# Performance work log

Hardware: AMD Instinct MI355X
Metric: run time of the kernel (lower is better)

## Reference

```python
import jax, jax.numpy as jnp
import numpy as np

B_SIZE = 4096
IN_FEATURES = 8192
OUT_FEATURES = IN_FEATURES + 6  # in + step(2) + 2*pad(2)
PAD = 2
BAND = 3  # each input column n contributes to output columns n..n+2


def setup_inputs() -> dict:
    key = jax.random.key(0)
    k1, k2, k3 = jax.random.split(key, 3)
    stdv = 1.0 / np.sqrt(IN_FEATURES)  # reset_parameters: uniform(-stdv, stdv)
    x = jax.random.normal(k1, (B_SIZE, IN_FEATURES), dtype=jnp.float32)
    weight = jax.random.uniform(k2, (OUT_FEATURES, IN_FEATURES), minval=-stdv, maxval=stdv, dtype=jnp.float32)
    bias = jax.random.uniform(k3, (OUT_FEATURES,), minval=-stdv, maxval=stdv, dtype=jnp.float32)
    return {"x": x, "weight": weight, "bias": bias}


def reference(x, weight, bias):
    # Torch loop: for n in range(F): out[:, n:n+3] += x[:, n:n+1] * weight[n:n+3, n] + bias[n:n+3]
    # => out[:, c] = sum_{n in [c-2, c] & [0, F)} x[:, n] * weight[c, n]  +  bias[c] * count(c)
    # where count(c) = number of valid n hitting column c (bias is re-added per touch).
    B, F = x.shape
    O = F + 2 * PAD + 2
    idx = jnp.arange(F)
    out = jnp.zeros((B, O), dtype=x.dtype)
    count = jnp.zeros((O,), dtype=x.dtype)
    for d in range(BAND):  # tiny fixed band, not a data-dim loop
        diag = weight[idx + d, idx]              # [F] band diagonal d
        out = out.at[:, d:d + F].add(x * diag[None, :])
        count = count.at[d:d + F].add(1.0)
    out = out + bias * count
    return out[:, PAD:-PAD]  # [B, F + 2]
```

## Files before the change

### kernel.cpp

```cpp
#include <hip/hip_runtime.h>

#define B_SIZE 4096
#define IN_F   8192
#define OUT_W  8194
#define ROWS_PER_BLOCK 16

__global__ __launch_bounds__(256) void coeff_kernel(
    const float* __restrict__ w, const float* __restrict__ bias,
    float4* __restrict__ coeff) {
  int j = blockIdx.x * blockDim.x + threadIdx.x;
  if (j >= OUT_W) return;
  size_t c = (size_t)j + 2;
  float c0 = 0.f, c1 = 0.f, c2 = 0.f, cnt = 0.f;
  if (j     < IN_F) { c0 = w[c * IN_F + j    ]; cnt += 1.f; }
  if (j + 1 < IN_F) { c1 = w[c * IN_F + j + 1]; cnt += 1.f; }
  if (j + 2 < IN_F) { c2 = w[c * IN_F + j + 2]; cnt += 1.f; }
  coeff[j] = make_float4(c0, c1, c2, cnt * bias[c]);
}

__global__ __launch_bounds__(256) void band_kernel(
    const float* __restrict__ x, const float4* __restrict__ coeff,
    float* __restrict__ out) {
  const int j = (blockIdx.x * 256 + threadIdx.x) * 4;
  const float4 k0 = coeff[j];
  const float4 k1 = coeff[j + 1];
  const float4 k2 = coeff[j + 2];
  const float4 k3 = coeff[j + 3];
  const bool g4 = (j + 4 < IN_F);
  const bool g5 = (j + 5 < IN_F);
  const bool tail = (blockIdx.x == gridDim.x - 1) && (threadIdx.x < 2);
  const int row0 = blockIdx.y * ROWS_PER_BLOCK;

  #pragma unroll 4
  for (int r = 0; r < ROWS_PER_BLOCK; ++r) {
    const size_t row = (size_t)(row0 + r);
    const float* xr = x + row * (size_t)IN_F;
    float4 xv = *reinterpret_cast<const float4*>(xr + j);
    float x4 = g4 ? xr[j + 4] : 0.f;
    float x5 = g5 ? xr[j + 5] : 0.f;
    float4 o;
    o.x = fmaf(k0.x, xv.x, fmaf(k0.y, xv.y, fmaf(k0.z, xv.z, k0.w)));
    o.y = fmaf(k1.x, xv.y, fmaf(k1.y, xv.z, fmaf(k1.z, xv.w, k1.w)));
    o.z = fmaf(k2.x, xv.z, fmaf(k2.y, xv.w, fmaf(k2.z, x4,  k2.w)));
    o.w = fmaf(k3.x, xv.w, fmaf(k3.y, x4,  fmaf(k3.z, x5,  k3.w)));
    float* orow = out + row * (size_t)OUT_W + j;
    reinterpret_cast<float2*>(orow)[0] = make_float2(o.x, o.y);
    reinterpret_cast<float2*>(orow)[1] = make_float2(o.z, o.w);
    if (tail) out[row * (size_t)OUT_W + 8192 + threadIdx.x] = 0.f;
  }
}

extern "C" void kernel_launch(void* const* d_in, const int* in_sizes, int n_in,
                              void* d_out, int out_size, void* d_ws, size_t ws_size,
                              hipStream_t stream) {
  const float* x    = (const float*)d_in[0];
  const float* w    = (const float*)d_in[1];
  const float* bias = (const float*)d_in[2];
  float* out = (float*)d_out;
  float4* coeff = (float4*)d_ws;

  coeff_kernel<<<(OUT_W + 255) / 256, 256, 0, stream>>>(w, bias, coeff);

  dim3 grid(8, B_SIZE / ROWS_PER_BLOCK);
  band_kernel<<<grid, 256, 0, stream>>>(x, coeff, out);
}
```

Before: 63.29 us.

## Fuse coefficient gather into band kernel, shuffle neighbors, double rows per block

```diff
diff --git a/kernel.cpp b/kernel.cpp
--- a/kernel.cpp
+++ b/kernel.cpp
@@ -3,50 +3,57 @@
 #define B_SIZE 4096
 #define IN_F   8192
 #define OUT_W  8194
-#define ROWS_PER_BLOCK 16
+#define ROWS   32
+#define CHUNKS 8
 
-__global__ __launch_bounds__(256) void coeff_kernel(
-    const float* __restrict__ w, const float* __restrict__ bias,
-    float4* __restrict__ coeff) {
-  int j = blockIdx.x * blockDim.x + threadIdx.x;
-  if (j >= OUT_W) return;
-  size_t c = (size_t)j + 2;
-  float c0 = 0.f, c1 = 0.f, c2 = 0.f, cnt = 0.f;
-  if (j     < IN_F) { c0 = w[c * IN_F + j    ]; cnt += 1.f; }
-  if (j + 1 < IN_F) { c1 = w[c * IN_F + j + 1]; cnt += 1.f; }
-  if (j + 2 < IN_F) { c2 = w[c * IN_F + j + 2]; cnt += 1.f; }
-  coeff[j] = make_float4(c0, c1, c2, cnt * bias[c]);
-}
+typedef float f32x4 __attribute__((ext_vector_type(4)));
+typedef float f32x2 __attribute__((ext_vector_type(2)));
 
-__global__ __launch_bounds__(256) void band_kernel(
-    const float* __restrict__ x, const float4* __restrict__ coeff,
-    float* __restrict__ out) {
-  const int j = (blockIdx.x * 256 + threadIdx.x) * 4;
-  const float4 k0 = coeff[j];
-  const float4 k1 = coeff[j + 1];
-  const float4 k2 = coeff[j + 2];
-  const float4 k3 = coeff[j + 3];
+__global__ __launch_bounds__(256) void glia_band_kernel(
+    const float* __restrict__ x, const float* __restrict__ w,
+    const float* __restrict__ bias, float* __restrict__ out) {
+  const int t = threadIdx.x;
+  const int j = (blockIdx.x * 256 + t) * 4;
+
+  float k[4][4];
+#pragma unroll
+  for (int q = 0; q < 4; ++q) {
+    const int jj = j + q;
+    const size_t c = (size_t)jj + 2;
+    float c1 = 0.f, c2 = 0.f, cnt = 1.f;
+    const float c0 = w[c * IN_F + jj];
+    if (jj + 1 < IN_F) { c1 = w[c * IN_F + jj + 1]; cnt += 1.f; }
+    if (jj + 2 < IN_F) { c2 = w[c * IN_F + jj + 2]; cnt += 1.f; }
+    k[q][0] = c0; k[q][1] = c1; k[q][2] = c2; k[q][3] = cnt * bias[c];
+  }
+
+  const int lane = t & 63;
+  const bool last_lane = (lane == 63);
   const bool g4 = (j + 4 < IN_F);
   const bool g5 = (j + 5 < IN_F);
-  const bool tail = (blockIdx.x == gridDim.x - 1) && (threadIdx.x < 2);
-  const int row0 = blockIdx.y * ROWS_PER_BLOCK;
+  const bool tail = (blockIdx.x == CHUNKS - 1) && (t == 255);
+  const int row0 = blockIdx.y * ROWS;
 
-  #pragma unroll 4
-  for (int r = 0; r < ROWS_PER_BLOCK; ++r) {
+#pragma unroll 4
+  for (int r = 0; r < ROWS; ++r) {
     const size_t row = (size_t)(row0 + r);
     const float* xr = x + row * (size_t)IN_F;
-    float4 xv = *reinterpret_cast<const float4*>(xr + j);
-    float x4 = g4 ? xr[j + 4] : 0.f;
-    float x5 = g5 ? xr[j + 5] : 0.f;
-    float4 o;
-    o.x = fmaf(k0.x, xv.x, fmaf(k0.y, xv.y, fmaf(k0.z, xv.z, k0.w)));
-    o.y = fmaf(k1.x, xv.y, fmaf(k1.y, xv.z, fmaf(k1.z, xv.w, k1.w)));
-    o.z = fmaf(k2.x, xv.z, fmaf(k2.y, xv.w, fmaf(k2.z, x4,  k2.w)));
-    o.w = fmaf(k3.x, xv.w, fmaf(k3.y, x4,  fmaf(k3.z, x5,  k3.w)));
+    const f32x4 xv = *reinterpret_cast<const f32x4*>(xr + j);
+    float x4 = __shfl_down(xv.x, 1);
+    float x5 = __shfl_down(xv.y, 1);
+    if (last_lane) {
+      x4 = g4 ? xr[j + 4] : 0.f;
+      x5 = g5 ? xr[j + 5] : 0.f;
+    }
+    const float o0 = fmaf(k[0][0], xv.x, fmaf(k[0][1], xv.y, fmaf(k[0][2], xv.z, k[0][3])));
+    const float o1 = fmaf(k[1][0], xv.y, fmaf(k[1][1], xv.z, fmaf(k[1][2], xv.w, k[1][3])));
+    const float o2 = fmaf(k[2][0], xv.z, fmaf(k[2][1], xv.w, fmaf(k[2][2], x4,   k[2][3])));
+    const float o3 = fmaf(k[3][0], xv.w, fmaf(k[3][1], x4,   fmaf(k[3][2], x5,   k[3][3])));
     float* orow = out + row * (size_t)OUT_W + j;
-    reinterpret_cast<float2*>(orow)[0] = make_float2(o.x, o.y);
-    reinterpret_cast<float2*>(orow)[1] = make_float2(o.z, o.w);
-    if (tail) out[row * (size_t)OUT_W + 8192 + threadIdx.x] = 0.f;
+    *reinterpret_cast<f32x2*>(orow)     = (f32x2){o0, o1};
+    *reinterpret_cast<f32x2*>(orow + 2) = (f32x2){o2, o3};
+    if (tail)
+      *reinterpret_cast<f32x2*>(out + row * (size_t)OUT_W + IN_F) = (f32x2){0.f, 0.f};
   }
 }
 
@@ -57,10 +64,7 @@
   const float* w    = (const float*)d_in[1];
   const float* bias = (const float*)d_in[2];
   float* out = (float*)d_out;
-  float4* coeff = (float4*)d_ws;
 
-  coeff_kernel<<<(OUT_W + 255) / 256, 256, 0, stream>>>(w, bias, coeff);
-
-  dim3 grid(8, B_SIZE / ROWS_PER_BLOCK);
-  band_kernel<<<grid, 256, 0, stream>>>(x, coeff, out);
+  dim3 grid(CHUNKS, B_SIZE / ROWS);
+  glia_band_kernel<<<grid, 256, 0, stream>>>(x, w, bias, out);
 }
```

Result: slower. 69.51 us (+9.8%).
